# Kernel optimization log

Hardware: AMD Instinct MI355X
Metric: run time of the kernel (lower is better)

The kernel has to match this reference:

```python
import jax, jax.numpy as jnp
import numpy as np

TEMPERATURE = 0.5
EPS = 1e-8  # torch CosineSimilarity eps


def setup_inputs() -> dict:
    key = jax.random.key(0)
    k1, k2 = jax.random.split(key)
    B, D = 4096, 256
    return {
        "z_i": jax.random.normal(k1, (B, D), dtype=jnp.float32),
        "z_j": jax.random.normal(k2, (B, D), dtype=jnp.float32),
    }


def reference(z_i, z_j):
    B = z_i.shape[0]
    N = 2 * B
    z = jnp.concatenate([z_i, z_j], axis=0)  # [N, D]
    # cosine similarity == normalized dot product (eps-clamped norms like torch)
    norms = jnp.maximum(jnp.linalg.norm(z, axis=1, keepdims=True), EPS)
    zn = z / norms
    sim = jnp.matmul(zn, zn.T) / TEMPERATURE  # [N, N]

    idx = jnp.arange(B)
    # positives: diag(sim, +B) and diag(sim, -B)
    pos = jnp.concatenate([sim[idx, idx + B], sim[idx + B, idx]])  # [N]

    # CrossEntropy with label 0 over [pos_i, negatives_i] reduces to
    # logsumexp over row i excluding the self-diagonal, minus pos_i.
    r = jnp.arange(N)
    neg_inf = jnp.finfo(sim.dtype).min
    sim_masked = jnp.where(r[:, None] == r[None, :], neg_inf, sim)
    lse = jax.nn.logsumexp(sim_masked, axis=1)  # [N]

    loss = (jnp.sum(lse) - jnp.sum(pos)) / N
    return loss
```

## Files before the change

kernel.cpp:

```cpp
#include <hip/hip_runtime.h>
#include <cstdint>

#define B_ROWS 4096
#define N_ROWS 8192
#define D_DIM  256
#define BT     128
#define TGRID  64
#define NTILES 2080
#define BK     32
#define NKT    8

typedef __attribute__((ext_vector_type(4))) float f32x4;
typedef __attribute__((ext_vector_type(8))) short bf16x8;
typedef __attribute__((ext_vector_type(4))) unsigned short u16x4;

__device__ __forceinline__ unsigned short f2bf(float f) {
    union { float f; unsigned u; } v; v.f = f;
    unsigned r = v.u + 0x7FFF + ((v.u >> 16) & 1);
    return (unsigned short)(r >> 16);
}
__device__ __forceinline__ float bf2f(unsigned short h) {
    union { unsigned u; float f; } v; v.u = ((unsigned)h) << 16;
    return v.f;
}

__device__ __forceinline__ void gload16(const void* g, void* l) {
    __builtin_amdgcn_global_load_lds(
        (const __attribute__((address_space(1))) void*)g,
        (__attribute__((address_space(3))) void*)l, 16, 0, 0);
}

__device__ __forceinline__ f32x4 exp4(f32x4 v) {
    f32x4 r;
    r.x = __expf(v.x); r.y = __expf(v.y); r.z = __expf(v.z); r.w = __expf(v.w);
    return r;
}

__global__ __launch_bounds__(256) void normpos_kernel(const float* __restrict__ zi,
                                                      const float* __restrict__ zj,
                                                      unsigned short* __restrict__ zn,
                                                      float* __restrict__ pospartial) {
    int wid = threadIdx.x >> 6;
    int lane = threadIdx.x & 63;
    int p = blockIdx.x * 4 + wid;
    f32x4 ga = *(const f32x4*)(zi + (size_t)p * D_DIM + lane * 4);
    f32x4 gb = *(const f32x4*)(zj + (size_t)p * D_DIM + lane * 4);
    float sa = ga.x * ga.x + ga.y * ga.y + ga.z * ga.z + ga.w * ga.w;
    float sb = gb.x * gb.x + gb.y * gb.y + gb.z * gb.z + gb.w * gb.w;
    #pragma unroll
    for (int m = 1; m < 64; m <<= 1) { sa += __shfl_xor(sa, m, 64); sb += __shfl_xor(sb, m, 64); }
    float fa = 1.41421356237309515f / fmaxf(sqrtf(sa), 1e-8f);
    float fb = 1.41421356237309515f / fmaxf(sqrtf(sb), 1e-8f);
    u16x4 oa, ob;
    oa.x = f2bf(ga.x * fa); oa.y = f2bf(ga.y * fa); oa.z = f2bf(ga.z * fa); oa.w = f2bf(ga.w * fa);
    ob.x = f2bf(gb.x * fb); ob.y = f2bf(gb.y * fb); ob.z = f2bf(gb.z * fb); ob.w = f2bf(gb.w * fb);
    *(u16x4*)(zn + (size_t)p * D_DIM + lane * 4) = oa;
    *(u16x4*)(zn + (size_t)(p + B_ROWS) * D_DIM + lane * 4) = ob;
    float d = bf2f(oa.x) * bf2f(ob.x) + bf2f(oa.y) * bf2f(ob.y)
            + bf2f(oa.z) * bf2f(ob.z) + bf2f(oa.w) * bf2f(ob.w);
    #pragma unroll
    for (int m = 1; m < 64; m <<= 1) d += __shfl_xor(d, m, 64);
    if (lane == 0) pospartial[p] = d;
}

__global__ __launch_bounds__(256, 3) void simclr_gemm_kernel(const unsigned short* __restrict__ zn,
                                                             float* __restrict__ P) {
    __shared__ unsigned short As[3][BT * BK];
    __shared__ unsigned short Bs[3][BT * BK];
    __shared__ float rPpart[2][BT];
    __shared__ float cPpart[2][BT];

    const int tid = threadIdx.x;
    const int lane = tid & 63, wid = tid >> 6;
    const int wr = wid >> 1, wc = wid & 1;

    int bid = (int)((blockIdx.x & 7) * (NTILES / 8) + (blockIdx.x >> 3));
    int ti = (int)((129.0f - sqrtf(16641.0f - 8.0f * (float)bid)) * 0.5f);
    while ((ti + 1) * TGRID - ((ti + 1) * ti) / 2 <= bid) ++ti;
    while (ti * TGRID - (ti * (ti - 1)) / 2 > bid) --ti;
    const int tj = ti + (bid - (ti * TGRID - (ti * (ti - 1)) / 2));

    const char* gA = (const char*)zn + (size_t)ti * BT * 512;
    const char* gB = (const char*)zn + (size_t)tj * BT * 512;

    const int r0 = tid >> 2, r1 = 64 + r0;
    const int sch = (tid & 3) ^ ((tid >> 3) & 3);
    const size_t gof0 = (size_t)r0 * 512 + (size_t)sch * 16;
    const size_t gof1 = (size_t)r1 * 512 + (size_t)sch * 16;
    const unsigned lo0 = (unsigned)tid * 8;
    const unsigned lo1 = 2048u + (unsigned)tid * 8;

    f32x4 acc[4][4];
    #pragma unroll
    for (int m = 0; m < 4; ++m)
        #pragma unroll
        for (int n = 0; n < 4; ++n)
            acc[m][n] = (f32x4){0.f, 0.f, 0.f, 0.f};

#define STAGE(buf_, kt_) do {                                     \
    size_t kb = (size_t)(kt_) * 64;                               \
    gload16(gA + gof0 + kb, &As[buf_][lo0]);                      \
    gload16(gA + gof1 + kb, &As[buf_][lo1]);                      \
    gload16(gB + gof0 + kb, &Bs[buf_][lo0]);                      \
    gload16(gB + gof1 + kb, &Bs[buf_][lo1]);                      \
} while (0)

    STAGE(0, 0);
    STAGE(1, 1);

    const int kc = (lane >> 4) ^ (((lane & 15) >> 1) & 3);
    const int arow = wr * 64 + (lane & 15);
    const int brow = wc * 64 + (lane & 15);

    #pragma unroll
    for (int kt = 0; kt < NKT; ++kt) {
        const int cur = kt % 3;
        if (kt < NKT - 1) asm volatile("s_waitcnt vmcnt(4)" ::: "memory");
        else              asm volatile("s_waitcnt vmcnt(0)" ::: "memory");
        __builtin_amdgcn_sched_barrier(0);
        __builtin_amdgcn_s_barrier();
        __builtin_amdgcn_sched_barrier(0);

        bf16x8 af[4], bfr[4];
        #pragma unroll
        for (int m = 0; m < 4; ++m)
            af[m] = *(const bf16x8*)&As[cur][(arow + m * 16) * 32 + kc * 8];
        #pragma unroll
        for (int n = 0; n < 4; ++n)
            bfr[n] = *(const bf16x8*)&Bs[cur][(brow + n * 16) * 32 + kc * 8];

        __builtin_amdgcn_s_setprio(1);
        #pragma unroll
        for (int m = 0; m < 4; ++m)
            #pragma unroll
            for (int n = 0; n < 4; ++n)
                acc[m][n] = __builtin_amdgcn_mfma_f32_16x16x32_bf16(af[m], bfr[n], acc[m][n], 0, 0, 0);
        __builtin_amdgcn_s_setprio(0);

        __builtin_amdgcn_sched_barrier(0);
        if (kt < NKT - 2) STAGE((kt + 2) % 3, kt + 2);
    }
#undef STAGE

    float cs[4] = {0.f, 0.f, 0.f, 0.f};
    #pragma unroll
    for (int m = 0; m < 4; ++m) {
        f32x4 ef[4];
        #pragma unroll
        for (int n = 0; n < 4; ++n) ef[n] = exp4(acc[m][n]);
        f32x4 rv = ef[0] + ef[1] + ef[2] + ef[3];
        #pragma unroll
        for (int msk = 1; msk <= 8; msk <<= 1) {
            rv.x += __shfl_xor(rv.x, msk, 64);
            rv.y += __shfl_xor(rv.y, msk, 64);
            rv.z += __shfl_xor(rv.z, msk, 64);
            rv.w += __shfl_xor(rv.w, msk, 64);
        }
        if ((lane & 15) == 0) {
            int rbase = wr * 64 + m * 16 + (lane >> 4) * 4;
            rPpart[wc][rbase + 0] = rv.x;
            rPpart[wc][rbase + 1] = rv.y;
            rPpart[wc][rbase + 2] = rv.z;
            rPpart[wc][rbase + 3] = rv.w;
        }
        #pragma unroll
        for (int n = 0; n < 4; ++n)
            cs[n] += ef[n].x + ef[n].y + ef[n].z + ef[n].w;
    }
    #pragma unroll
    for (int n = 0; n < 4; ++n) {
        float c = cs[n];
        c += __shfl_xor(c, 16, 64);
        c += __shfl_xor(c, 32, 64);
        if (lane < 16) cPpart[wr][wc * 64 + n * 16 + lane] = c;
    }
    __syncthreads();

    if (tid < BT) {
        P[(size_t)tj * N_ROWS + ti * BT + tid] = rPpart[0][tid] + rPpart[1][tid];
    } else if (ti != tj) {
        int t = tid - BT;
        P[(size_t)ti * N_ROWS + tj * BT + t] = cPpart[0][t] + cPpart[1][t];
    }
}

__global__ __launch_bounds__(256) void reduce_rows_kernel(const float* __restrict__ P,
                                                          const float* __restrict__ pospartial,
                                                          float* __restrict__ blockpart) {
    const float E2 = 7.38905609893065f;
    int row = blockIdx.x * 256 + threadIdx.x;
    float s = 0.f;
    #pragma unroll 16
    for (int src = 0; src < TGRID; ++src)
        s += P[(size_t)src * N_ROWS + row];
    float v = logf(s - E2);
    if (threadIdx.x < 128)
        v -= 2.0f * pospartial[blockIdx.x * 128 + threadIdx.x];
    #pragma unroll
    for (int m = 1; m < 64; m <<= 1) v += __shfl_xor(v, m, 64);
    __shared__ float ws[4];
    if ((threadIdx.x & 63) == 0) ws[threadIdx.x >> 6] = v;
    __syncthreads();
    if (threadIdx.x == 0) blockpart[blockIdx.x] = ws[0] + ws[1] + ws[2] + ws[3];
}

__global__ __launch_bounds__(64) void final_kernel(const float* __restrict__ blockpart,
                                                   float* __restrict__ out) {
    int lane = threadIdx.x;
    float v = (lane < 32) ? blockpart[lane] : 0.f;
    #pragma unroll
    for (int m = 1; m < 64; m <<= 1) v += __shfl_xor(v, m, 64);
    if (lane == 0) out[0] = v / (float)N_ROWS;
}

extern "C" void kernel_launch(void* const* d_in, const int* in_sizes, int n_in,
                              void* d_out, int out_size, void* d_ws, size_t ws_size,
                              hipStream_t stream) {
    const float* zi = (const float*)d_in[0];
    const float* zj = (const float*)d_in[1];
    char* ws = (char*)d_ws;
    unsigned short* zn = (unsigned short*)ws;
    float* P = (float*)(ws + 4 * 1024 * 1024);
    float* pospartial = (float*)(ws + 6 * 1024 * 1024);
    float* blockpart = (float*)(ws + 6 * 1024 * 1024 + 16 * 1024);

    normpos_kernel<<<B_ROWS / 4, 256, 0, stream>>>(zi, zj, zn, pospartial);
    simclr_gemm_kernel<<<NTILES, 256, 0, stream>>>(zn, P);
    reduce_rows_kernel<<<N_ROWS / 256, 256, 0, stream>>>(P, pospartial, blockpart);
    final_kernel<<<1, 64, 0, stream>>>(blockpart, (float*)d_out);
}
```

Before: 45.65 us.

## Use 256x128 rectangular tiles over the upper-triangular sim matrix

Replaces the 128x128 symmetric tile grid with 256x128 tiles, where each block covers a 256-row panel against a 128-column panel. This cuts the block count and roughly halves redundant A-panel loads. The partial-sum layout changes so that column sums go to extra P rows, and the reduction kernel is updated to match. In exchange, register pressure rises (32 accumulators per wave), occupancy drops to 2 blocks, and the diagonal handling wastes some work on half-masked tiles.

```diff
diff --git a/kernel.cpp b/kernel.cpp
--- a/kernel.cpp
+++ b/kernel.cpp
@@ -4,9 +4,9 @@
 #define B_ROWS 4096
 #define N_ROWS 8192
 #define D_DIM  256
-#define BT     128
 #define TGRID  64
-#define NTILES 2080
+#define TIPS   32
+#define NBLOCKS 1056
 #define BK     32
 #define NKT    8
 
@@ -63,67 +63,68 @@
     if (lane == 0) pospartial[p] = d;
 }
 
-__global__ __launch_bounds__(256, 3) void simclr_gemm_kernel(const unsigned short* __restrict__ zn,
+__global__ __launch_bounds__(256, 2) void simclr_gemm_kernel(const unsigned short* __restrict__ zn,
                                                              float* __restrict__ P) {
-    __shared__ unsigned short As[3][BT * BK];
-    __shared__ unsigned short Bs[3][BT * BK];
-    __shared__ float rPpart[2][BT];
-    __shared__ float cPpart[2][BT];
+    __shared__ unsigned short As[3][256 * BK];
+    __shared__ unsigned short Bs[3][128 * BK];
+    __shared__ float rPpart[2][256];
+    __shared__ float cPpart[2][128];
 
     const int tid = threadIdx.x;
     const int lane = tid & 63, wid = tid >> 6;
     const int wr = wid >> 1, wc = wid & 1;
 
-    int bid = (int)((blockIdx.x & 7) * (NTILES / 8) + (blockIdx.x >> 3));
-    int ti = (int)((129.0f - sqrtf(16641.0f - 8.0f * (float)bid)) * 0.5f);
-    while ((ti + 1) * TGRID - ((ti + 1) * ti) / 2 <= bid) ++ti;
-    while (ti * TGRID - (ti * (ti - 1)) / 2 > bid) --ti;
-    const int tj = ti + (bid - (ti * TGRID - (ti * (ti - 1)) / 2));
-
-    const char* gA = (const char*)zn + (size_t)ti * BT * 512;
-    const char* gB = (const char*)zn + (size_t)tj * BT * 512;
-
-    const int r0 = tid >> 2, r1 = 64 + r0;
+    int bid = (int)((blockIdx.x & 7) * (NBLOCKS / 8) + (blockIdx.x >> 3));
+    int tip = (int)((65.0f - sqrtf(4225.0f - 4.0f * (float)bid)) * 0.5f);
+    if (tip > 31) tip = 31;
+    while ((tip + 1) * (65 - (tip + 1)) <= bid) ++tip;
+    while (tip * (65 - tip) > bid) --tip;
+    const int tj = 2 * tip + (bid - tip * (65 - tip));
+
+    const char* gA = (const char*)zn + (size_t)tip * 256 * 512;
+    const char* gB = (const char*)zn + (size_t)tj * 128 * 512;
+
+    const int r0 = tid >> 2;
     const int sch = (tid & 3) ^ ((tid >> 3) & 3);
-    const size_t gof0 = (size_t)r0 * 512 + (size_t)sch * 16;
-    const size_t gof1 = (size_t)r1 * 512 + (size_t)sch * 16;
-    const unsigned lo0 = (unsigned)tid * 8;
-    const unsigned lo1 = 2048u + (unsigned)tid * 8;
-
-    f32x4 acc[4][4];
-    #pragma unroll
-    for (int m = 0; m < 4; ++m)
+    const size_t gbase = (size_t)r0 * 512 + (size_t)sch * 16;
+    const unsigned lo = (unsigned)tid * 8;
+
+    f32x4 acc[8][4];
+    #pragma unroll
+    for (int m = 0; m < 8; ++m)
         #pragma unroll
         for (int n = 0; n < 4; ++n)
             acc[m][n] = (f32x4){0.f, 0.f, 0.f, 0.f};
 
-#define STAGE(buf_, kt_) do {                                     \
-    size_t kb = (size_t)(kt_) * 64;                               \
-    gload16(gA + gof0 + kb, &As[buf_][lo0]);                      \
-    gload16(gA + gof1 + kb, &As[buf_][lo1]);                      \
-    gload16(gB + gof0 + kb, &Bs[buf_][lo0]);                      \
-    gload16(gB + gof1 + kb, &Bs[buf_][lo1]);                      \
+#define STAGE(buf_, kt_) do {                                         \
+    size_t kb = (size_t)(kt_) * 64;                                   \
+    gload16(gA + gbase + kb,              &As[buf_][lo]);             \
+    gload16(gA + gbase + 64 * 512 + kb,   &As[buf_][2048u + lo]);     \
+    gload16(gA + gbase + 128 * 512 + kb,  &As[buf_][4096u + lo]);     \
+    gload16(gA + gbase + 192 * 512 + kb,  &As[buf_][6144u + lo]);     \
+    gload16(gB + gbase + kb,              &Bs[buf_][lo]);             \
+    gload16(gB + gbase + 64 * 512 + kb,   &Bs[buf_][2048u + lo]);     \
 } while (0)
 
     STAGE(0, 0);
     STAGE(1, 1);
 
     const int kc = (lane >> 4) ^ (((lane & 15) >> 1) & 3);
-    const int arow = wr * 64 + (lane & 15);
+    const int arow = wr * 128 + (lane & 15);
     const int brow = wc * 64 + (lane & 15);
 
     #pragma unroll
     for (int kt = 0; kt < NKT; ++kt) {
         const int cur = kt % 3;
-        if (kt < NKT - 1) asm volatile("s_waitcnt vmcnt(4)" ::: "memory");
+        if (kt < NKT - 1) asm volatile("s_waitcnt vmcnt(6)" ::: "memory");
         else              asm volatile("s_waitcnt vmcnt(0)" ::: "memory");
         __builtin_amdgcn_sched_barrier(0);
         __builtin_amdgcn_s_barrier();
         __builtin_amdgcn_sched_barrier(0);
 
-        bf16x8 af[4], bfr[4];
-        #pragma unroll
-        for (int m = 0; m < 4; ++m)
+        bf16x8 af[8], bfr[4];
+        #pragma unroll
+        for (int m = 0; m < 8; ++m)
             af[m] = *(const bf16x8*)&As[cur][(arow + m * 16) * 32 + kc * 8];
         #pragma unroll
         for (int n = 0; n < 4; ++n)
@@ -131,7 +132,7 @@
 
         __builtin_amdgcn_s_setprio(1);
         #pragma unroll
-        for (int m = 0; m < 4; ++m)
+        for (int m = 0; m < 8; ++m)
             #pragma unroll
             for (int n = 0; n < 4; ++n)
                 acc[m][n] = __builtin_amdgcn_mfma_f32_16x16x32_bf16(af[m], bfr[n], acc[m][n], 0, 0, 0);
@@ -144,7 +145,7 @@
 
     float cs[4] = {0.f, 0.f, 0.f, 0.f};
     #pragma unroll
-    for (int m = 0; m < 4; ++m) {
+    for (int m = 0; m < 8; ++m) {
         f32x4 ef[4];
         #pragma unroll
         for (int n = 0; n < 4; ++n) ef[n] = exp4(acc[m][n]);
@@ -157,7 +158,7 @@
             rv.w += __shfl_xor(rv.w, msk, 64);
         }
         if ((lane & 15) == 0) {
-            int rbase = wr * 64 + m * 16 + (lane >> 4) * 4;
+            int rbase = wr * 128 + m * 16 + (lane >> 4) * 4;
             rPpart[wc][rbase + 0] = rv.x;
             rPpart[wc][rbase + 1] = rv.y;
             rPpart[wc][rbase + 2] = rv.z;
@@ -176,11 +177,15 @@
     }
     __syncthreads();
 
-    if (tid < BT) {
-        P[(size_t)tj * N_ROWS + ti * BT + tid] = rPpart[0][tid] + rPpart[1][tid];
-    } else if (ti != tj) {
-        int t = tid - BT;
-        P[(size_t)ti * N_ROWS + tj * BT + t] = cPpart[0][t] + cPpart[1][t];
+    {
+        float rs = rPpart[0][tid] + rPpart[1][tid];
+        if (tj == 2 * tip && tid >= 128) rs = 0.f;
+        P[(size_t)tj * N_ROWS + (size_t)tip * 256 + tid] = rs;
+    }
+    if (tid < 128) {
+        float s0 = (tj > 2 * tip)     ? cPpart[0][tid] : 0.f;
+        float s1 = (tj > 2 * tip + 1) ? cPpart[1][tid] : 0.f;
+        P[(size_t)(64 + tip) * N_ROWS + (size_t)tj * 128 + tid] = s0 + s1;
     }
 }
 
@@ -189,10 +194,15 @@
                                                           float* __restrict__ blockpart) {
     const float E2 = 7.38905609893065f;
     int row = blockIdx.x * 256 + threadIdx.x;
+    int tip = row >> 8;
+    int tjr = row >> 7;
     float s = 0.f;
-    #pragma unroll 16
-    for (int src = 0; src < TGRID; ++src)
+    #pragma unroll 4
+    for (int src = 2 * tip; src < TGRID; ++src)
         s += P[(size_t)src * N_ROWS + row];
+    #pragma unroll 4
+    for (int sc = 0; sc <= (tjr >> 1); ++sc)
+        s += P[(size_t)(64 + sc) * N_ROWS + row];
     float v = logf(s - E2);
     if (threadIdx.x < 128)
         v -= 2.0f * pospartial[blockIdx.x * 128 + threadIdx.x];
@@ -207,7 +217,7 @@
 __global__ __launch_bounds__(64) void final_kernel(const float* __restrict__ blockpart,
                                                    float* __restrict__ out) {
     int lane = threadIdx.x;
-    float v = (lane < 32) ? blockpart[lane] : 0.f;
+    float v = (lane < TIPS) ? blockpart[lane] : 0.f;
     #pragma unroll
     for (int m = 1; m < 64; m <<= 1) v += __shfl_xor(v, m, 64);
     if (lane == 0) out[0] = v / (float)N_ROWS;
@@ -221,11 +231,11 @@
     char* ws = (char*)d_ws;
     unsigned short* zn = (unsigned short*)ws;
     float* P = (float*)(ws + 4 * 1024 * 1024);
-    float* pospartial = (float*)(ws + 6 * 1024 * 1024);
-    float* blockpart = (float*)(ws + 6 * 1024 * 1024 + 16 * 1024);
+    float* pospartial = (float*)(ws + 8 * 1024 * 1024);
+    float* blockpart = (float*)(ws + 8 * 1024 * 1024 + 16 * 1024);
 
     normpos_kernel<<<B_ROWS / 4, 256, 0, stream>>>(zi, zj, zn, pospartial);
-    simclr_gemm_kernel<<<NTILES, 256, 0, stream>>>(zn, P);
-    reduce_rows_kernel<<<N_ROWS / 256, 256, 0, stream>>>(P, pospartial, blockpart);
+    simclr_gemm_kernel<<<NBLOCKS, 256, 0, stream>>>(zn, P);
+    reduce_rows_kernel<<<TIPS, 256, 0, stream>>>(P, pospartial, blockpart);
     final_kernel<<<1, 64, 0, stream>>>(blockpart, (float*)d_out);
 }
```

Result: slower. 50.32 us (+10.2%).

## Keep A row-panel resident in registers and sweep four B tiles per block

Applied to the files above, without the earlier changes.

Each block now loads its 128-row A panel once (all 8 K-slices) into registers and iterates over up to four upper-triangular column tiles, streaming only B slices through a 3-buffer LDS ring. The grid shrinks from 2080 one-tile blocks to 544 multi-tile blocks, cutting redundant A loads and per-block launch/index overhead. It costs more registers (occupancy bound lowered to 2) and longer serial per-block work with fewer blocks, which may hurt load balance across CUs.

```diff
diff --git a/kernel.cpp b/kernel.cpp
--- a/kernel.cpp
+++ b/kernel.cpp
@@ -4,9 +4,9 @@
 #define B_ROWS 4096
 #define N_ROWS 8192
 #define D_DIM  256
-#define BT     128
 #define TGRID  64
-#define NTILES 2080
+#define NJ     4
+#define NBLOCKS 544
 #define BK     32
 #define NKT    8
 
@@ -63,125 +63,155 @@
     if (lane == 0) pospartial[p] = d;
 }
 
-__global__ __launch_bounds__(256, 3) void simclr_gemm_kernel(const unsigned short* __restrict__ zn,
+__global__ __launch_bounds__(256, 2) void simclr_gemm_kernel(const unsigned short* __restrict__ zn,
                                                              float* __restrict__ P) {
-    __shared__ unsigned short As[3][BT * BK];
-    __shared__ unsigned short Bs[3][BT * BK];
-    __shared__ float rPpart[2][BT];
-    __shared__ float cPpart[2][BT];
+    __shared__ unsigned short SH[33792];
+    float* rPpart = (float*)&SH[32768];
+    float* cPpart = rPpart + 256;
 
     const int tid = threadIdx.x;
     const int lane = tid & 63, wid = tid >> 6;
     const int wr = wid >> 1, wc = wid & 1;
 
-    int bid = (int)((blockIdx.x & 7) * (NTILES / 8) + (blockIdx.x >> 3));
-    int ti = (int)((129.0f - sqrtf(16641.0f - 8.0f * (float)bid)) * 0.5f);
-    while ((ti + 1) * TGRID - ((ti + 1) * ti) / 2 <= bid) ++ti;
-    while (ti * TGRID - (ti * (ti - 1)) / 2 > bid) --ti;
-    const int tj = ti + (bid - (ti * TGRID - (ti * (ti - 1)) / 2));
-
-    const char* gA = (const char*)zn + (size_t)ti * BT * 512;
-    const char* gB = (const char*)zn + (size_t)tj * BT * 512;
-
-    const int r0 = tid >> 2, r1 = 64 + r0;
+    int bid = (int)((blockIdx.x & 7) * (NBLOCKS / 8) + (blockIdx.x >> 3));
+    int ti = 0, cum = 0;
+    for (;;) {
+        int c = (TGRID - ti + 3) >> 2;
+        if (bid < cum + c) break;
+        cum += c; ++ti;
+    }
+    const int jc = bid - cum;
+    const int j0 = ti + 4 * jc;
+    const int nj = min(NJ, TGRID - j0);
+    const int G = nj * NKT;
+
+    const char* gA = (const char*)zn + (size_t)ti * 128 * 512;
+
+    const int r0 = tid >> 2;
     const int sch = (tid & 3) ^ ((tid >> 3) & 3);
-    const size_t gof0 = (size_t)r0 * 512 + (size_t)sch * 16;
-    const size_t gof1 = (size_t)r1 * 512 + (size_t)sch * 16;
+    const size_t gbase = (size_t)r0 * 512 + (size_t)sch * 16;
     const unsigned lo0 = (unsigned)tid * 8;
     const unsigned lo1 = 2048u + (unsigned)tid * 8;
 
-    f32x4 acc[4][4];
-    #pragma unroll
-    for (int m = 0; m < 4; ++m)
-        #pragma unroll
-        for (int n = 0; n < 4; ++n)
-            acc[m][n] = (f32x4){0.f, 0.f, 0.f, 0.f};
-
-#define STAGE(buf_, kt_) do {                                     \
-    size_t kb = (size_t)(kt_) * 64;                               \
-    gload16(gA + gof0 + kb, &As[buf_][lo0]);                      \
-    gload16(gA + gof1 + kb, &As[buf_][lo1]);                      \
-    gload16(gB + gof0 + kb, &Bs[buf_][lo0]);                      \
-    gload16(gB + gof1 + kb, &Bs[buf_][lo1]);                      \
-} while (0)
-
-    STAGE(0, 0);
-    STAGE(1, 1);
+    #pragma unroll
+    for (int s = 0; s < 8; ++s) {
+        gload16(gA + gbase + s * 64,            &SH[s * 4096 + lo0]);
+        gload16(gA + gbase + 64 * 512 + s * 64, &SH[s * 4096 + lo1]);
+    }
+    asm volatile("s_waitcnt vmcnt(0)" ::: "memory");
+    __builtin_amdgcn_sched_barrier(0);
+    __builtin_amdgcn_s_barrier();
+    __builtin_amdgcn_sched_barrier(0);
 
     const int kc = (lane >> 4) ^ (((lane & 15) >> 1) & 3);
     const int arow = wr * 64 + (lane & 15);
     const int brow = wc * 64 + (lane & 15);
 
-    #pragma unroll
-    for (int kt = 0; kt < NKT; ++kt) {
-        const int cur = kt % 3;
-        if (kt < NKT - 1) asm volatile("s_waitcnt vmcnt(4)" ::: "memory");
-        else              asm volatile("s_waitcnt vmcnt(0)" ::: "memory");
+    bf16x8 af[4][8];
+    #pragma unroll
+    for (int kt = 0; kt < 8; ++kt)
+        #pragma unroll
+        for (int m = 0; m < 4; ++m)
+            af[m][kt] = *(const bf16x8*)&SH[kt * 4096 + (arow + m * 16) * 32 + kc * 8];
+    asm volatile("s_waitcnt lgkmcnt(0)" ::: "memory");
+    __builtin_amdgcn_sched_barrier(0);
+    __builtin_amdgcn_s_barrier();
+    __builtin_amdgcn_sched_barrier(0);
+
+#define STAGE_B(h_) do {                                                       \
+    int jt_ = (h_) >> 3, kt_ = (h_) & 7, b_ = (h_) % 3;                        \
+    const char* gBp = (const char*)zn + (size_t)(j0 + jt_) * 128 * 512;        \
+    gload16(gBp + gbase + kt_ * 64,            &SH[b_ * 4096 + lo0]);          \
+    gload16(gBp + gbase + 64 * 512 + kt_ * 64, &SH[b_ * 4096 + lo1]);          \
+} while (0)
+
+    STAGE_B(0);
+    STAGE_B(1);
+
+    f32x4 acc[4][4];
+    #pragma unroll
+    for (int m = 0; m < 4; ++m)
+        #pragma unroll
+        for (int n = 0; n < 4; ++n)
+            acc[m][n] = (f32x4){0.f, 0.f, 0.f, 0.f};
+
+    for (int jt = 0; jt < nj; ++jt) {
+        const int tj = j0 + jt;
+        #pragma unroll
+        for (int kt = 0; kt < 8; ++kt) {
+            const int g = jt * 8 + kt;
+            if (g == G - 1) asm volatile("s_waitcnt vmcnt(0)" ::: "memory");
+            else            asm volatile("s_waitcnt vmcnt(2)" ::: "memory");
+            __builtin_amdgcn_sched_barrier(0);
+            __builtin_amdgcn_s_barrier();
+            __builtin_amdgcn_sched_barrier(0);
+
+            const int b = (2 * jt + kt) % 3;
+            bf16x8 bfr[4];
+            #pragma unroll
+            for (int n = 0; n < 4; ++n)
+                bfr[n] = *(const bf16x8*)&SH[b * 4096 + (brow + n * 16) * 32 + kc * 8];
+
+            __builtin_amdgcn_s_setprio(1);
+            #pragma unroll
+            for (int m = 0; m < 4; ++m)
+                #pragma unroll
+                for (int n = 0; n < 4; ++n)
+                    acc[m][n] = __builtin_amdgcn_mfma_f32_16x16x32_bf16(af[m][kt], bfr[n], acc[m][n], 0, 0, 0);
+            __builtin_amdgcn_s_setprio(0);
+
+            __builtin_amdgcn_sched_barrier(0);
+            if (g + 2 < G) STAGE_B(g + 2);
+        }
+
+        float cs[4] = {0.f, 0.f, 0.f, 0.f};
+        #pragma unroll
+        for (int m = 0; m < 4; ++m) {
+            f32x4 ef[4];
+            #pragma unroll
+            for (int n = 0; n < 4; ++n) ef[n] = exp4(acc[m][n]);
+            #pragma unroll
+            for (int n = 0; n < 4; ++n)
+                acc[m][n] = (f32x4){0.f, 0.f, 0.f, 0.f};
+            f32x4 rv = ef[0] + ef[1] + ef[2] + ef[3];
+            #pragma unroll
+            for (int msk = 1; msk <= 8; msk <<= 1) {
+                rv.x += __shfl_xor(rv.x, msk, 64);
+                rv.y += __shfl_xor(rv.y, msk, 64);
+                rv.z += __shfl_xor(rv.z, msk, 64);
+                rv.w += __shfl_xor(rv.w, msk, 64);
+            }
+            if ((lane & 15) == 0) {
+                int rbase = wr * 64 + m * 16 + (lane >> 4) * 4;
+                rPpart[wc * 128 + rbase + 0] = rv.x;
+                rPpart[wc * 128 + rbase + 1] = rv.y;
+                rPpart[wc * 128 + rbase + 2] = rv.z;
+                rPpart[wc * 128 + rbase + 3] = rv.w;
+            }
+            #pragma unroll
+            for (int n = 0; n < 4; ++n)
+                cs[n] += ef[n].x + ef[n].y + ef[n].z + ef[n].w;
+        }
+        #pragma unroll
+        for (int n = 0; n < 4; ++n) {
+            float c = cs[n];
+            c += __shfl_xor(c, 16, 64);
+            c += __shfl_xor(c, 32, 64);
+            if (lane < 16) cPpart[wr * 128 + wc * 64 + n * 16 + lane] = c;
+        }
+        asm volatile("s_waitcnt lgkmcnt(0)" ::: "memory");
         __builtin_amdgcn_sched_barrier(0);
         __builtin_amdgcn_s_barrier();
         __builtin_amdgcn_sched_barrier(0);
 
-        bf16x8 af[4], bfr[4];
-        #pragma unroll
-        for (int m = 0; m < 4; ++m)
-            af[m] = *(const bf16x8*)&As[cur][(arow + m * 16) * 32 + kc * 8];
-        #pragma unroll
-        for (int n = 0; n < 4; ++n)
-            bfr[n] = *(const bf16x8*)&Bs[cur][(brow + n * 16) * 32 + kc * 8];
-
-        __builtin_amdgcn_s_setprio(1);
-        #pragma unroll
-        for (int m = 0; m < 4; ++m)
-            #pragma unroll
-            for (int n = 0; n < 4; ++n)
-                acc[m][n] = __builtin_amdgcn_mfma_f32_16x16x32_bf16(af[m], bfr[n], acc[m][n], 0, 0, 0);
-        __builtin_amdgcn_s_setprio(0);
-
-        __builtin_amdgcn_sched_barrier(0);
-        if (kt < NKT - 2) STAGE((kt + 2) % 3, kt + 2);
+        if (tid < 128) {
+            P[(size_t)tj * N_ROWS + (size_t)ti * 128 + tid] = rPpart[tid] + rPpart[128 + tid];
+        } else if (tj != ti) {
+            int t = tid - 128;
+            P[(size_t)ti * N_ROWS + (size_t)tj * 128 + t] = cPpart[t] + cPpart[128 + t];
+        }
     }
-#undef STAGE
-
-    float cs[4] = {0.f, 0.f, 0.f, 0.f};
-    #pragma unroll
-    for (int m = 0; m < 4; ++m) {
-        f32x4 ef[4];
-        #pragma unroll
-        for (int n = 0; n < 4; ++n) ef[n] = exp4(acc[m][n]);
-        f32x4 rv = ef[0] + ef[1] + ef[2] + ef[3];
-        #pragma unroll
-        for (int msk = 1; msk <= 8; msk <<= 1) {
-            rv.x += __shfl_xor(rv.x, msk, 64);
-            rv.y += __shfl_xor(rv.y, msk, 64);
-            rv.z += __shfl_xor(rv.z, msk, 64);
-            rv.w += __shfl_xor(rv.w, msk, 64);
-        }
-        if ((lane & 15) == 0) {
-            int rbase = wr * 64 + m * 16 + (lane >> 4) * 4;
-            rPpart[wc][rbase + 0] = rv.x;
-            rPpart[wc][rbase + 1] = rv.y;
-            rPpart[wc][rbase + 2] = rv.z;
-            rPpart[wc][rbase + 3] = rv.w;
-        }
-        #pragma unroll
-        for (int n = 0; n < 4; ++n)
-            cs[n] += ef[n].x + ef[n].y + ef[n].z + ef[n].w;
-    }
-    #pragma unroll
-    for (int n = 0; n < 4; ++n) {
-        float c = cs[n];
-        c += __shfl_xor(c, 16, 64);
-        c += __shfl_xor(c, 32, 64);
-        if (lane < 16) cPpart[wr][wc * 64 + n * 16 + lane] = c;
-    }
-    __syncthreads();
-
-    if (tid < BT) {
-        P[(size_t)tj * N_ROWS + ti * BT + tid] = rPpart[0][tid] + rPpart[1][tid];
-    } else if (ti != tj) {
-        int t = tid - BT;
-        P[(size_t)ti * N_ROWS + tj * BT + t] = cPpart[0][t] + cPpart[1][t];
-    }
+#undef STAGE_B
 }
 
 __global__ __launch_bounds__(256) void reduce_rows_kernel(const float* __restrict__ P,
@@ -225,7 +255,7 @@
     float* blockpart = (float*)(ws + 6 * 1024 * 1024 + 16 * 1024);
 
     normpos_kernel<<<B_ROWS / 4, 256, 0, stream>>>(zi, zj, zn, pospartial);
-    simclr_gemm_kernel<<<NTILES, 256, 0, stream>>>(zn, P);
+    simclr_gemm_kernel<<<NBLOCKS, 256, 0, stream>>>(zn, P);
     reduce_rows_kernel<<<N_ROWS / 256, 256, 0, stream>>>(P, pospartial, blockpart);
     final_kernel<<<1, 64, 0, stream>>>(blockpart, (float*)d_out);
 }
```

Result: slower. 59.38 us (+30.1%).
